# Performance work log

Hardware: AMD Instinct MI355X
Metric: run time of the kernel (lower is better)

Reference implementation:

```python
import jax, jax.numpy as jnp
import numpy as np

NEG = -9e15
SLOPE = 0.1  # LeakyReLU negative_slope in the torch module

B, N, NFEAT = 4, 2048, 256
NHID, NHEADS, NOUT = 64, 8, 128


def setup_inputs() -> dict:
    key = jax.random.key(0)
    ks = jax.random.split(key, 8)
    x = jax.random.normal(ks[0], (B, N, NFEAT), dtype=jnp.float32)
    adj = jax.random.randint(ks[1], (B, N, N), 0, 2, dtype=jnp.int32)
    s = 0.1
    Wh = jax.random.normal(ks[2], (NHEADS, NFEAT, NHID), dtype=jnp.float32) * s
    ah = jax.random.normal(ks[3], (NHEADS, 2 * NHID), dtype=jnp.float32) * s
    bh = jax.random.normal(ks[4], (NHEADS, NHID), dtype=jnp.float32) * s
    Wo = jax.random.normal(ks[5], (NHID * NHEADS, NOUT), dtype=jnp.float32) * s
    ao = jax.random.normal(ks[6], (2 * NOUT,), dtype=jnp.float32) * s
    bo = jax.random.normal(ks[7], (NOUT,), dtype=jnp.float32) * s
    return {"x": x, "adj": adj, "Wh": Wh, "ah": ah, "bh": bh,
            "Wo": Wo, "ao": ao, "bo": bo}


def _leaky(v):
    return jnp.where(v >= 0, v, SLOPE * v)


def _gat_layer(x, adj, W, a, b):
    # x: [B,N,Fin], W: [Fin,F], a: [2F], b: [F]
    h = jnp.einsum('bnf,fo->bno', x, W)          # [B,N,F]
    F = W.shape[1]
    a1, a2 = a[:F], a[F:]
    s1 = h @ a1                                   # [B,N] (query / row term)
    s2 = h @ a2                                   # [B,N] (key / col term)
    e = _leaky(s1[:, :, None] + s2[:, None, :])   # [B,N,N], avoids a_input blowup
    e = jnp.where(adj > 0, e, NEG)
    att = jax.nn.softmax(e, axis=2)               # [B,N,N]
    h_prime = jnp.einsum('bnm,bmf->bnf', att, h) + b
    return jax.nn.elu(h_prime)


def reference(x, adj, Wh, ah, bh, Wo, ao, bo):
    # per-head layers, vmapped over the head axis of the stacked params
    heads = jax.vmap(lambda W, a, b: _gat_layer(x, adj, W, a, b))(Wh, ah, bh)
    # [H,B,N,F] -> concat heads along feature dim: [B,N,H*F]
    hcat = jnp.transpose(heads, (1, 2, 0, 3)).reshape(x.shape[0], x.shape[1], -1)
    out = _gat_layer(hcat, adj, Wo, ao, bo)
    return jax.nn.relu(out)
```

## Files before the change

### kernel.cpp

```cpp
#include <hip/hip_runtime.h>

constexpr int B_ = 4;
constexpr int N_ = 2048;
constexpr int NFEAT_ = 256;
constexpr int NHEADS_ = 8;
constexpr float SLOPE_ = 0.1f;
constexpr float L2E = 1.4426950408889634f;

typedef __attribute__((ext_vector_type(8))) __fp16 f16x8;
typedef __attribute__((ext_vector_type(4))) __fp16 f16x4;
typedef __attribute__((ext_vector_type(2))) __fp16 f16x2;
typedef __attribute__((ext_vector_type(4))) float f32x4;
typedef __attribute__((ext_vector_type(2))) float f32x2;

__device__ __forceinline__ f16x8 pack8(const float* v) {
  union { f16x2 h2[4]; f16x8 h8; } u;
  u.h2[0] = __builtin_amdgcn_cvt_pkrtz(v[0], v[1]);
  u.h2[1] = __builtin_amdgcn_cvt_pkrtz(v[2], v[3]);
  u.h2[2] = __builtin_amdgcn_cvt_pkrtz(v[4], v[5]);
  u.h2[3] = __builtin_amdgcn_cvt_pkrtz(v[6], v[7]);
  return u.h8;
}
__device__ __forceinline__ f16x4 pack4(float a, float b, float c, float d) {
  union { f16x2 h2[2]; f16x4 h4; } u;
  u.h2[0] = __builtin_amdgcn_cvt_pkrtz(a, b);
  u.h2[1] = __builtin_amdgcn_cvt_pkrtz(c, d);
  return u.h4;
}

__device__ __forceinline__ unsigned int wpair(f32x2 p2, f32x2 s2p,
                                              f16x2 sl2, f16x2 cq2,
                                              unsigned int pm) {
  f32x2 z;
  asm("v_pk_add_f32 %0, %1, %2" : "=v"(z) : "v"(p2), "v"(s2p));
  f16x2 t0 = __builtin_amdgcn_cvt_pkrtz(z.x, z.y);
  f16x2 t1, tm;
  asm("v_pk_fma_f16 %0, %1, %2, %3" : "=v"(t1) : "v"(sl2), "v"(t0), "v"(cq2));
  asm("v_pk_max_f16 %0, %1, %2" : "=v"(tm) : "v"(t0), "v"(t1));
  unsigned int utm;
  __builtin_memcpy(&utm, &tm, 4);
  unsigned int hi, elo, ehi, pk;
  asm("v_lshrrev_b32 %0, 16, %1" : "=v"(hi) : "v"(utm));
  asm("v_exp_f16 %0, %1" : "=v"(elo) : "v"(utm));
  asm("v_exp_f16 %0, %1" : "=v"(ehi) : "v"(hi));
  asm("v_pack_b32_f16 %0, %1, %2" : "=v"(pk) : "v"(elo), "v"(ehi));
  return pk & pm;
}

__global__ __launch_bounds__(256) void k_prep(
    const int* __restrict__ adj, unsigned short* __restrict__ mask2,
    const float* __restrict__ Wh, __fp16* __restrict__ WhB,
    const float* __restrict__ Wo, __fp16* __restrict__ WoB)
{
  const int bid = blockIdx.x;
  const int l = threadIdx.x & 63;
  if (bid < 4096) {
    const size_t gw = ((size_t)bid * 256 + threadIdx.x) >> 6;
    const int jt = (int)(gw & 31);
    const int ig16 = (int)((gw >> 5) & 127);
    const int b = (int)(gw >> 12);
    const int q = l >> 4, c15 = l & 15;
    const int* base = adj + ((size_t)b * N_ + ig16 * 16) * N_ + jt * 64 + l;
    unsigned int msk = 0;
    #pragma unroll
    for (int r = 0; r < 16; ++r) {
      int a = base[(size_t)r * N_];
      unsigned long long bal = __ballot(a > 0);
      unsigned int v = (unsigned int)((bal >> (q * 8)) & 0xffull)
                     | ((unsigned int)((bal >> (q * 8 + 32)) & 0xffull) << 8);
      if (r == c15) msk = v;
    }
    mask2[gw * 64 + l] = (unsigned short)msk;
  } else if (bid < 4160) {
    int s = (int)(((bid - 4096) * 256 + threadIdx.x) >> 6);
    int h = s >> 5, ks = (s >> 2) & 7, ft = s & 3;
    const float* src = Wh + ((size_t)h * 256 + ks * 32 + (l >> 4) * 8) * 64 + ft * 16 + (l & 15);
    float v[8];
    #pragma unroll
    for (int j = 0; j < 8; ++j) v[j] = src[(size_t)j * 64];
    *(f16x8*)(WhB + (size_t)s * 512 + l * 8) = pack8(v);
  } else {
    int s = (int)(((bid - 4160) * 256 + threadIdx.x) >> 6);
    int ks = s >> 3, ft = s & 7;
    const float* src = Wo + ((size_t)ks * 32 + (l >> 4) * 8) * 128 + ft * 16 + (l & 15);
    float v[8];
    #pragma unroll
    for (int j = 0; j < 8; ++j) v[j] = src[(size_t)j * 128];
    *(f16x8*)(WoB + (size_t)s * 512 + l * 8) = pack8(v);
  }
}

__global__ __launch_bounds__(256, 4) void k_gemm1(
    const float* __restrict__ x, const __fp16* __restrict__ WhB,
    const float* __restrict__ ah,
    __fp16* __restrict__ hB1, float* __restrict__ s1h, float* __restrict__ s2h)
{
  constexpr int XP = 264;
  __shared__ __fp16 xs[16 * XP];
  __shared__ __fp16 hT[512 * 16];

  const int t = threadIdx.x;
  const int bid = blockIdx.x;
  const int b = bid >> 7;
  const int n0 = (bid & 127) * 16;

  {
    int r = t >> 4, k0 = (t & 15) * 16;
    const float* src = x + ((size_t)(b * N_) + n0 + r) * NFEAT_ + k0;
    float v0[8], v1[8];
    *(float4*)&v0[0] = *(const float4*)(src);
    *(float4*)&v0[4] = *(const float4*)(src + 4);
    *(float4*)&v1[0] = *(const float4*)(src + 8);
    *(float4*)&v1[4] = *(const float4*)(src + 12);
    *(f16x8*)&xs[r * XP + k0] = pack8(v0);
    *(f16x8*)&xs[r * XP + k0 + 8] = pack8(v1);
  }
  __syncthreads();

  const int w = t >> 6, l = t & 63;
  const int quad = l >> 4, c15 = l & 15;

  f32x4 acc[8];
  #pragma unroll
  for (int i = 0; i < 8; ++i) acc[i] = (f32x4){0.f, 0.f, 0.f, 0.f};

  for (int ks = 0; ks < 8; ++ks) {
    f16x8 af = *(const f16x8*)&xs[c15 * XP + ks * 32 + quad * 8];
    #pragma unroll
    for (int tt = 0; tt < 8; ++tt) {
      int hl = tt >> 2, ft = tt & 3;
      f16x8 bf = *(const f16x8*)(WhB +
          ((((size_t)(2 * w + hl) * 8 + ks) * 4 + ft) * 512) + l * 8);
      acc[tt] = __builtin_amdgcn_mfma_f32_16x16x32_f16(af, bf, acc[tt], 0, 0, 0);
    }
  }

  #pragma unroll
  for (int hl = 0; hl < 2; ++hl) {
    int head = 2 * w + hl;
    float a1v[4], a2v[4];
    #pragma unroll
    for (int ft = 0; ft < 4; ++ft) {
      a1v[ft] = ah[head * 128 + ft * 16 + c15] * L2E;
      a2v[ft] = ah[head * 128 + 64 + ft * 16 + c15] * L2E;
    }
    #pragma unroll
    for (int r = 0; r < 4; ++r) {
      float v1 = 0.f, v2 = 0.f;
      #pragma unroll
      for (int ft = 0; ft < 4; ++ft) {
        v1 = fmaf(acc[hl * 4 + ft][r], a1v[ft], v1);
        v2 = fmaf(acc[hl * 4 + ft][r], a2v[ft], v2);
      }
      #pragma unroll
      for (int off = 1; off < 16; off <<= 1) {
        v1 += __shfl_xor(v1, off, 64);
        v2 += __shfl_xor(v2, off, 64);
      }
      if (c15 == 0) {
        s1h[(size_t)(b * NHEADS_ + head) * N_ + n0 + quad * 4 + r] = v1;
        s2h[(size_t)(b * NHEADS_ + head) * N_ + n0 + quad * 4 + r] = v2;
      }
    }
  }

  #pragma unroll
  for (int tt = 0; tt < 8; ++tt) {
    int f = (2 * w + (tt >> 2)) * 64 + (tt & 3) * 16 + c15;
    *(f16x4*)&hT[f * 16 + quad * 4] =
        pack4(acc[tt][0], acc[tt][1], acc[tt][2], acc[tt][3]);
  }
  __syncthreads();

  const int base_oct = (n0 >> 3) & 3;
  #pragma unroll
  for (int q = 0; q < 4; ++q) {
    int s = t + q * 256;
    int c15v = s & 15, oct = (s >> 4) & 1, ft = (s >> 5) & 3, head = s >> 7;
    f16x8 v = *(const f16x8*)&hT[(head * 64 + ft * 16 + c15v) * 16 + oct * 8];
    int lane0 = (base_oct + oct) * 16 + c15v;
    *(f16x8*)(hB1 +
        ((((size_t)(b * NHEADS_ + head) * 64 + (n0 >> 5)) * 4 + ft) * 512) + lane0 * 8) = v;
  }
}

__global__ __launch_bounds__(256, 4) void k_gemm2(
    const __fp16* __restrict__ g1, const __fp16* __restrict__ WoB,
    const float* __restrict__ ao,
    __fp16* __restrict__ hB2, float* __restrict__ s1o, float* __restrict__ s2o)
{
  constexpr int GP = 520;
  __shared__ __fp16 gs[16 * GP];
  __shared__ __fp16 hT[128 * 16];
  __shared__ float sd1[4][16], sd2[4][16];

  const int t = threadIdx.x;
  const int bid = blockIdx.x;
  const int b = bid >> 7;
  const int n0 = (bid & 127) * 16;

  {
    int r = t >> 4, k0 = (t & 15) * 32;
    const __fp16* src = g1 + ((size_t)(b * N_) + n0 + r) * 512 + k0;
    #pragma unroll
    for (int i = 0; i < 4; ++i)
      *(f16x8*)&gs[r * GP + k0 + i * 8] = *(const f16x8*)(src + i * 8);
  }
  __syncthreads();

  const int w = t >> 6, l = t & 63;
  const int quad = l >> 4, c15 = l & 15;

  f32x4 acc[2];
  acc[0] = (f32x4){0.f, 0.f, 0.f, 0.f};
  acc[1] = (f32x4){0.f, 0.f, 0.f, 0.f};

  for (int ks = 0; ks < 16; ++ks) {
    f16x8 af = *(const f16x8*)&gs[c15 * GP + ks * 32 + quad * 8];
    #pragma unroll
    for (int tt = 0; tt < 2; ++tt) {
      int ft = 2 * w + tt;
      f16x8 bf = *(const f16x8*)(WoB + (((size_t)ks * 8 + ft) * 512) + l * 8);
      acc[tt] = __builtin_amdgcn_mfma_f32_16x16x32_f16(af, bf, acc[tt], 0, 0, 0);
    }
  }

  {
    float a1v[2], a2v[2];
    #pragma unroll
    for (int tt = 0; tt < 2; ++tt) {
      int f = (2 * w + tt) * 16 + c15;
      a1v[tt] = ao[f] * L2E;
      a2v[tt] = ao[128 + f] * L2E;
    }
    #pragma unroll
    for (int r = 0; r < 4; ++r) {
      float v1 = acc[0][r] * a1v[0] + acc[1][r] * a1v[1];
      float v2 = acc[0][r] * a2v[0] + acc[1][r] * a2v[1];
      #pragma unroll
      for (int off = 1; off < 16; off <<= 1) {
        v1 += __shfl_xor(v1, off, 64);
        v2 += __shfl_xor(v2, off, 64);
      }
      if (c15 == 0) { sd1[w][quad * 4 + r] = v1; sd2[w][quad * 4 + r] = v2; }
    }
  }

  #pragma unroll
  for (int tt = 0; tt < 2; ++tt) {
    int f = (2 * w + tt) * 16 + c15;
    *(f16x4*)&hT[f * 16 + quad * 4] =
        pack4(acc[tt][0], acc[tt][1], acc[tt][2], acc[tt][3]);
  }
  __syncthreads();

  if (t < 16)
    s1o[(size_t)b * N_ + n0 + t] = sd1[0][t] + sd1[1][t] + sd1[2][t] + sd1[3][t];
  else if (t < 32) {
    int rr = t - 16;
    s2o[(size_t)b * N_ + n0 + rr] = sd2[0][rr] + sd2[1][rr] + sd2[2][rr] + sd2[3][rr];
  }

  {
    int c15v = t & 15, oct = (t >> 4) & 1, ft = t >> 5;
    f16x8 v = *(const f16x8*)&hT[(ft * 16 + c15v) * 16 + oct * 8];
    int base_oct = (n0 >> 3) & 3;
    int lane0 = (base_oct + oct) * 16 + c15v;
    *(f16x8*)(hB2 +
        (((size_t)(b * 64 + (n0 >> 5)) * 8 + ft) * 512) + lane0 * 8) = v;
  }
}

__global__ __launch_bounds__(512, 4) void k_att1(
    const __fp16* __restrict__ hB, const float* __restrict__ s1,
    const float* __restrict__ s2, const unsigned short* __restrict__ mask2,
    const float* __restrict__ bias, __fp16* __restrict__ g1)
{
  constexpr int NRG = 4, NJQ = 2, JLEN = 1024, TJ = 32, NIT = JLEN / TJ;
  constexpr int TILE = TJ * 64;

  __shared__ __fp16 vbuf[NJQ][2][TILE];
  __shared__ float s2s[N_];
  __shared__ float red[8];
  __shared__ uint2 mlut[16];

  const int tid = threadIdx.x;
  const int w = tid >> 6, l = tid & 63;
  const int quad = l >> 4, c15 = l & 15;
  const int rowg = w % NRG, jq = w / NRG;
  const int tc = rowg * 64 + l;

  int idx = blockIdx.x;
  const int ig = idx & 31; idx >>= 5;
  const int head = idx & 7;
  const int b = idx >> 3;
  const int i0w = ig * 64 + rowg * 16;

  const float* s1p = s1 + (size_t)(b * 8 + head) * N_;
  const float* s2p = s2 + (size_t)(b * 8 + head) * N_;
  const char* hBp = (const char*)(hB + (size_t)(b * 8 + head) * (N_ / 32) * 2048);
  const unsigned short* mp = mask2 + ((size_t)(b * 128 + (i0w >> 4)) * 32) * 64 + l;

  const int jbase = jq * JLEN;

  if (tid < 16) {
    unsigned int v = tid;
    mlut[tid] = (uint2){ ((v & 1u) ? 0xffffu : 0u) | ((v & 2u) ? 0xffff0000u : 0u),
                         ((v & 4u) ? 0xffffu : 0u) | ((v & 8u) ? 0xffff0000u : 0u) };
  }

  float4 pf0 = *(const float4*)(hBp + (size_t)(jbase >> 5) * 4096 + tc * 16);
  unsigned short mk = mp[(size_t)(jbase >> 6) * 64];

  float4 sv = *(const float4*)(s2p + tid * 4);
  *(float4*)&s2s[tid * 4] = sv;
  float lm = fmaxf(fmaxf(sv.x, sv.y), fmaxf(sv.z, sv.w));
  #pragma unroll
  for (int off = 1; off < 64; off <<= 1) lm = fmaxf(lm, __shfl_xor(lm, off, 64));
  if (l == 0) red[w] = lm;
  const float s1v = s1p[i0w + c15];
  *(float4*)((char*)&vbuf[jq][0][0] + tc * 16) = pf0;
  __syncthreads();
  float s2m = red[0];
  #pragma unroll
  for (int q = 1; q < 8; ++q) s2m = fmaxf(s2m, red[q]);

  const float zm = s1v + s2m;
  const float m = fmaxf(zm, SLOPE_ * zm);
  const float p = s1v - m;
  const float cq = (SLOPE_ - 1.f) * m;
  const f16x2 cq2 = __builtin_amdgcn_cvt_pkrtz(cq, cq);
  const f16x2 sl2 = (f16x2){(__fp16)SLOPE_, (__fp16)SLOPE_};
  const f32x2 p2 = {p, p};

  f16x8 ones;
  #pragma unroll
  for (int i = 0; i < 8; ++i) ones[i] = (__fp16)1.0f;

  f32x4 acc[4], acc5;
  #pragma unroll
  for (int t = 0; t < 4; ++t) acc[t] = (f32x4){0.f, 0.f, 0.f, 0.f};
  acc5 = (f32x4){0.f, 0.f, 0.f, 0.f};

  for (int it = 0; it < NIT; ++it) {
    const int cur = it & 1;
    const int j0 = jbase + it * TJ;
    unsigned short nk = 0;
    float4 npf;
    if (it + 1 < NIT) {
      npf = *(const float4*)(hBp + (size_t)((j0 + TJ) >> 5) * 4096 + tc * 16);
      nk = mp[(size_t)((j0 + TJ) >> 6) * 64];
    }

    float4 sA = *(const float4*)&s2s[j0 + quad * 8];
    float4 sB = *(const float4*)&s2s[j0 + quad * 8 + 4];
    const unsigned int mbyte = ((unsigned int)mk >> (8 * ((j0 >> 5) & 1))) & 0xffu;
    const uint2 mA = mlut[mbyte & 15u];
    const uint2 mB = mlut[mbyte >> 4];
    union { unsigned int u[4]; f16x8 v8; } af;
    af.u[0] = wpair(p2, (f32x2){sA.x, sA.y}, sl2, cq2, mA.x);
    af.u[1] = wpair(p2, (f32x2){sA.z, sA.w}, sl2, cq2, mA.y);
    af.u[2] = wpair(p2, (f32x2){sB.x, sB.y}, sl2, cq2, mB.x);
    af.u[3] = wpair(p2, (f32x2){sB.z, sB.w}, sl2, cq2, mB.y);
    const f16x8 a = af.v8;
    acc5 = __builtin_amdgcn_mfma_f32_16x16x32_f16(a, ones, acc5, 0, 0, 0);
    const __fp16* vb = &vbuf[jq][cur][0];
    #pragma unroll
    for (int t = 0; t < 4; ++t) {
      f16x8 bf = *(const f16x8*)(vb + t * 512 + l * 8);
      acc[t] = __builtin_amdgcn_mfma_f32_16x16x32_f16(a, bf, acc[t], 0, 0, 0);
    }

    if (it + 1 < NIT) {
      *(float4*)((char*)&vbuf[jq][cur ^ 1][0] + tc * 16) = npf;
    }
    mk = nk;
    __syncthreads();
  }

  auto pacc = (float(*)[16][64])(&vbuf[0][0][0]);
  auto pls  = (float(*)[16])(&s2s[0]);
  if (jq == 1) {
    #pragma unroll
    for (int t = 0; t < 4; ++t)
      #pragma unroll
      for (int r = 0; r < 4; ++r)
        pacc[rowg][quad * 4 + r][t * 16 + c15] = acc[t][r];
    if (c15 == 0) {
      #pragma unroll
      for (int r = 0; r < 4; ++r) pls[rowg][quad * 4 + r] = acc5[r];
    }
  }
  __syncthreads();
  if (jq == 0) {
    float Lrow[4];
    #pragma unroll
    for (int r = 0; r < 4; ++r)
      Lrow[r] = acc5[r] + pls[rowg][quad * 4 + r];
    #pragma unroll
    for (int t = 0; t < 4; ++t)
      #pragma unroll
      for (int r = 0; r < 4; ++r)
        acc[t][r] += pacc[rowg][quad * 4 + r][t * 16 + c15];
    float lr[4];
    #pragma unroll
    for (int r = 0; r < 4; ++r) lr[r] = 1.f / Lrow[r];
    #pragma unroll
    for (int t = 0; t < 4; ++t) {
      const float bv = bias[head * 64 + t * 16 + c15];
      #pragma unroll
      for (int r = 0; r < 4; ++r) {
        const int i = i0w + quad * 4 + r;
        float v = acc[t][r] * lr[r] + bv;
        v = (v > 0.f) ? v : expm1f(v);
        g1[(size_t)(b * N_ + i) * 512 + head * 64 + t * 16 + c15] = (__fp16)v;
      }
    }
  }
}

__global__ __launch_bounds__(512, 4) void k_att2(
    const __fp16* __restrict__ hB, const float* __restrict__ s1,
    const float* __restrict__ s2, const unsigned short* __restrict__ mask2,
    const float* __restrict__ bias, float* __restrict__ out)
{
  constexpr int NRG = 2, NJQ = 4, JLEN = 512, TJ = 32, NIT = JLEN / TJ;
  constexpr int TILE = TJ * 64;

  __shared__ __fp16 vbuf[NJQ][2][TILE];
  __shared__ float s2s[N_];
  __shared__ float red[8];
  __shared__ uint2 mlut[16];

  const int tid = threadIdx.x;
  const int w = tid >> 6, l = tid & 63;
  const int quad = l >> 4, c15 = l & 15;
  const int rowg = w % NRG, jq = w / NRG;
  const int tc = rowg * 64 + l;

  int idx = blockIdx.x;
  const int ig = idx & 63; idx >>= 6;
  const int fs = idx & 1;
  const int b = idx >> 1;
  const int i0w = ig * 32 + rowg * 16;

  const float* s1p = s1 + (size_t)b * N_;
  const float* s2p = s2 + (size_t)b * N_;
  const char* hBp = (const char*)(hB + (size_t)b * 64 * 4096 + fs * 2048);
  const unsigned short* mp = mask2 + ((size_t)(b * 128 + (i0w >> 4)) * 32) * 64 + l;

  const int jbase = jq * JLEN;

  if (tid < 16) {
    unsigned int v = tid;
    mlut[tid] = (uint2){ ((v & 1u) ? 0xffffu : 0u) | ((v & 2u) ? 0xffff0000u : 0u),
                         ((v & 4u) ? 0xffffu : 0u) | ((v & 8u) ? 0xffff0000u : 0u) };
  }

  float4 pf0, pf1;
  {
    const char* srcb = hBp + (size_t)(jbase >> 5) * 8192;
    pf0 = *(const float4*)(srcb + tc * 16);
    pf1 = *(const float4*)(srcb + (tc + 128) * 16);
  }
  unsigned short mk = mp[(size_t)(jbase >> 6) * 64];

  float4 sv = *(const float4*)(s2p + tid * 4);
  *(float4*)&s2s[tid * 4] = sv;
  float lm = fmaxf(fmaxf(sv.x, sv.y), fmaxf(sv.z, sv.w));
  #pragma unroll
  for (int off = 1; off < 64; off <<= 1) lm = fmaxf(lm, __shfl_xor(lm, off, 64));
  if (l == 0) red[w] = lm;
  const float s1v = s1p[i0w + c15];
  *(float4*)((char*)&vbuf[jq][0][0] + tc * 16) = pf0;
  *(float4*)((char*)&vbuf[jq][0][0] + (tc + 128) * 16) = pf1;
  __syncthreads();
  float s2m = red[0];
  #pragma unroll
  for (int q = 1; q < 8; ++q) s2m = fmaxf(s2m, red[q]);

  const float zm = s1v + s2m;
  const float m = fmaxf(zm, SLOPE_ * zm);
  const float p = s1v - m;
  const float cq = (SLOPE_ - 1.f) * m;
  const f16x2 cq2 = __builtin_amdgcn_cvt_pkrtz(cq, cq);
  const f16x2 sl2 = (f16x2){(__fp16)SLOPE_, (__fp16)SLOPE_};
  const f32x2 p2 = {p, p};

  f16x8 ones;
  #pragma unroll
  for (int i = 0; i < 8; ++i) ones[i] = (__fp16)1.0f;

  f32x4 acc[4], acc5;
  #pragma unroll
  for (int t = 0; t < 4; ++t) acc[t] = (f32x4){0.f, 0.f, 0.f, 0.f};
  acc5 = (f32x4){0.f, 0.f, 0.f, 0.f};

  for (int it = 0; it < NIT; ++it) {
    const int cur = it & 1;
    const int j0 = jbase + it * TJ;
    unsigned short nk = 0;
    float4 npf0, npf1;
    if (it + 1 < NIT) {
      const char* srcb = hBp + (size_t)((j0 + TJ) >> 5) * 8192;
      npf0 = *(const float4*)(srcb + tc * 16);
      npf1 = *(const float4*)(srcb + (tc + 128) * 16);
      nk = mp[(size_t)((j0 + TJ) >> 6) * 64];
    }

    float4 sA = *(const float4*)&s2s[j0 + quad * 8];
    float4 sB = *(const float4*)&s2s[j0 + quad * 8 + 4];
    const unsigned int mbyte = ((unsigned int)mk >> (8 * ((j0 >> 5) & 1))) & 0xffu;
    const uint2 mA = mlut[mbyte & 15u];
    const uint2 mB = mlut[mbyte >> 4];
    union { unsigned int u[4]; f16x8 v8; } af;
    af.u[0] = wpair(p2, (f32x2){sA.x, sA.y}, sl2, cq2, mA.x);
    af.u[1] = wpair(p2, (f32x2){sA.z, sA.w}, sl2, cq2, mA.y);
    af.u[2] = wpair(p2, (f32x2){sB.x, sB.y}, sl2, cq2, mB.x);
    af.u[3] = wpair(p2, (f32x2){sB.z, sB.w}, sl2, cq2, mB.y);
    const f16x8 a = af.v8;
    acc5 = __builtin_amdgcn_mfma_f32_16x16x32_f16(a, ones, acc5, 0, 0, 0);
    const __fp16* vb = &vbuf[jq][cur][0];
    #pragma unroll
    for (int t = 0; t < 4; ++t) {
      f16x8 bf = *(const f16x8*)(vb + t * 512 + l * 8);
      acc[t] = __builtin_amdgcn_mfma_f32_16x16x32_f16(a, bf, acc[t], 0, 0, 0);
    }

    if (it + 1 < NIT) {
      char* dst = (char*)&vbuf[jq][cur ^ 1][0];
      *(float4*)(dst + tc * 16) = npf0;
      *(float4*)(dst + (tc + 128) * 16) = npf1;
    }
    mk = nk;
    __syncthreads();
  }

  auto pacc = (float(*)[NRG][16][64])(&vbuf[0][0][0]);
  auto pls  = (float(*)[NRG][16])(&s2s[0]);
  if (jq > 0) {
    #pragma unroll
    for (int t = 0; t < 4; ++t)
      #pragma unroll
      for (int r = 0; r < 4; ++r)
        pacc[jq - 1][rowg][quad * 4 + r][t * 16 + c15] = acc[t][r];
    if (c15 == 0) {
      #pragma unroll
      for (int r = 0; r < 4; ++r) pls[jq - 1][rowg][quad * 4 + r] = acc5[r];
    }
  }
  __syncthreads();
  if (jq == 0) {
    float Lrow[4];
    #pragma unroll
    for (int r = 0; r < 4; ++r) Lrow[r] = acc5[r];
    #pragma unroll
    for (int q = 0; q < NJQ - 1; ++q) {
      #pragma unroll
      for (int t = 0; t < 4; ++t)
        #pragma unroll
        for (int r = 0; r < 4; ++r)
          acc[t][r] += pacc[q][rowg][quad * 4 + r][t * 16 + c15];
      #pragma unroll
      for (int r = 0; r < 4; ++r) Lrow[r] += pls[q][rowg][quad * 4 + r];
    }
    float lr[4];
    #pragma unroll
    for (int r = 0; r < 4; ++r) lr[r] = 1.f / Lrow[r];
    #pragma unroll
    for (int t = 0; t < 4; ++t) {
      const float bv = bias[fs * 64 + t * 16 + c15];
      #pragma unroll
      for (int r = 0; r < 4; ++r) {
        const int i = i0w + quad * 4 + r;
        float v = acc[t][r] * lr[r] + bv;
        out[(size_t)(b * N_ + i) * 128 + fs * 64 + t * 16 + c15] = fmaxf(v, 0.f);
      }
    }
  }
}

extern "C" void kernel_launch(void* const* d_in, const int* in_sizes, int n_in,
                              void* d_out, int out_size, void* d_ws, size_t ws_size,
                              hipStream_t stream) {
  const float* x   = (const float*)d_in[0];
  const int*   adj = (const int*)d_in[1];
  const float* Wh  = (const float*)d_in[2];
  const float* ah  = (const float*)d_in[3];
  const float* bh  = (const float*)d_in[4];
  const float* Wo  = (const float*)d_in[5];
  const float* ao  = (const float*)d_in[6];
  const float* bo  = (const float*)d_in[7];
  float* out = (float*)d_out;

  float* ws   = (float*)d_ws;
  float* s1h  = ws;
  float* s2h  = s1h  + (size_t)B_ * NHEADS_ * N_;
  float* s1o  = s2h  + (size_t)B_ * NHEADS_ * N_;
  float* s2o  = s1o  + (size_t)B_ * N_;
  __fp16* g1  = (__fp16*)(s2o + (size_t)B_ * N_);
  __fp16* hB1 = g1  + (size_t)B_ * N_ * 512;
  __fp16* hB2 = hB1 + (size_t)B_ * NHEADS_ * N_ * 64;
  __fp16* WhB = hB2 + (size_t)B_ * N_ * 128;
  __fp16* WoB = WhB + (size_t)8 * 256 * 64;
  unsigned short* mask2 = (unsigned short*)(WoB + (size_t)512 * 128);

  k_prep<<<4192, 256, 0, stream>>>(adj, mask2, Wh, WhB, Wo, WoB);
  k_gemm1<<<B_ * (N_ / 16), 256, 0, stream>>>(x, WhB, ah, hB1, s1h, s2h);
  k_att1<<<B_ * NHEADS_ * (N_ / 64), 512, 0, stream>>>(
      hB1, s1h, s2h, mask2, bh, g1);
  k_gemm2<<<B_ * (N_ / 16), 256, 0, stream>>>(g1, WoB, ao, hB2, s1o, s2o);
  k_att2<<<B_ * 2 * (N_ / 32), 512, 0, stream>>>(
      hB2, s1o, s2o, mask2, bo, out);
}
```

Baseline: 194.0 us.

## Load attention value tiles directly from global into registers, drop LDS staging

Both attention kernels stop staging the hB value tiles through double-buffered shared memory with a barrier per tile. Each wave now loads its MFMA B-operands straight from global memory into registers, two tiles at a time with software prefetch. In k_att1 each wave covers the full key range for 16 rows, so the cross-wave reduction is gone and the grid is halved with 128 rows per block. This removes LDS traffic and __syncthreads stalls, but makes each wave re-read the same hB data from global/L2 and gives up the split-K parallelism in att1.

```diff
diff --git a/kernel.cpp b/kernel.cpp
--- a/kernel.cpp
+++ b/kernel.cpp
@@ -276,10 +276,8 @@
     const float* __restrict__ s2, const unsigned short* __restrict__ mask2,
     const float* __restrict__ bias, __fp16* __restrict__ g1)
 {
-  constexpr int NRG = 4, NJQ = 2, JLEN = 1024, TJ = 32, NIT = JLEN / TJ;
-  constexpr int TILE = TJ * 64;
-
-  __shared__ __fp16 vbuf[NJQ][2][TILE];
+  constexpr int NPR = N_ / 64;
+
   __shared__ float s2s[N_];
   __shared__ float red[8];
   __shared__ uint2 mlut[16];
@@ -287,21 +285,24 @@
   const int tid = threadIdx.x;
   const int w = tid >> 6, l = tid & 63;
   const int quad = l >> 4, c15 = l & 15;
-  const int rowg = w % NRG, jq = w / NRG;
-  const int tc = rowg * 64 + l;
 
   int idx = blockIdx.x;
-  const int ig = idx & 31; idx >>= 5;
+  const int ig = idx & 15; idx >>= 4;
   const int head = idx & 7;
   const int b = idx >> 3;
-  const int i0w = ig * 64 + rowg * 16;
+  const int i0w = ig * 128 + w * 16;
 
   const float* s1p = s1 + (size_t)(b * 8 + head) * N_;
   const float* s2p = s2 + (size_t)(b * 8 + head) * N_;
-  const char* hBp = (const char*)(hB + (size_t)(b * 8 + head) * (N_ / 32) * 2048);
+  const char* hBl = (const char*)(hB + (size_t)(b * 8 + head) * (N_ / 32) * 2048)
+                    + l * 16;
   const unsigned short* mp = mask2 + ((size_t)(b * 128 + (i0w >> 4)) * 32) * 64 + l;
 
-  const int jbase = jq * JLEN;
+  f16x8 bA[4], bB[4];
+  #pragma unroll
+  for (int t = 0; t < 4; ++t)
+    bA[t] = *(const f16x8*)(hBl + t * 1024);
+  unsigned short mk = mp[0];
 
   if (tid < 16) {
     unsigned int v = tid;
@@ -309,9 +310,6 @@
                          ((v & 4u) ? 0xffffu : 0u) | ((v & 8u) ? 0xffff0000u : 0u) };
   }
 
-  float4 pf0 = *(const float4*)(hBp + (size_t)(jbase >> 5) * 4096 + tc * 16);
-  unsigned short mk = mp[(size_t)(jbase >> 6) * 64];
-
   float4 sv = *(const float4*)(s2p + tid * 4);
   *(float4*)&s2s[tid * 4] = sv;
   float lm = fmaxf(fmaxf(sv.x, sv.y), fmaxf(sv.z, sv.w));
@@ -319,7 +317,6 @@
   for (int off = 1; off < 64; off <<= 1) lm = fmaxf(lm, __shfl_xor(lm, off, 64));
   if (l == 0) red[w] = lm;
   const float s1v = s1p[i0w + c15];
-  *(float4*)((char*)&vbuf[jq][0][0] + tc * 16) = pf0;
   __syncthreads();
   float s2m = red[0];
   #pragma unroll
@@ -342,79 +339,67 @@
   for (int t = 0; t < 4; ++t) acc[t] = (f32x4){0.f, 0.f, 0.f, 0.f};
   acc5 = (f32x4){0.f, 0.f, 0.f, 0.f};
 
-  for (int it = 0; it < NIT; ++it) {
-    const int cur = it & 1;
-    const int j0 = jbase + it * TJ;
+  for (int pr = 0; pr < NPR; ++pr) {
+    const int j0 = pr * 64;
+    #pragma unroll
+    for (int t = 0; t < 4; ++t)
+      bB[t] = *(const f16x8*)(hBl + (size_t)(j0 / 32 + 1) * 4096 + t * 1024);
+    {
+      float4 sA = *(const float4*)&s2s[j0 + quad * 8];
+      float4 sB = *(const float4*)&s2s[j0 + quad * 8 + 4];
+      const unsigned int mbyte = (unsigned int)mk & 0xffu;
+      const uint2 mA = mlut[mbyte & 15u];
+      const uint2 mH = mlut[mbyte >> 4];
+      union { unsigned int u[4]; f16x8 v8; } af;
+      af.u[0] = wpair(p2, (f32x2){sA.x, sA.y}, sl2, cq2, mA.x);
+      af.u[1] = wpair(p2, (f32x2){sA.z, sA.w}, sl2, cq2, mA.y);
+      af.u[2] = wpair(p2, (f32x2){sB.x, sB.y}, sl2, cq2, mH.x);
+      af.u[3] = wpair(p2, (f32x2){sB.z, sB.w}, sl2, cq2, mH.y);
+      const f16x8 a = af.v8;
+      acc5 = __builtin_amdgcn_mfma_f32_16x16x32_f16(a, ones, acc5, 0, 0, 0);
+      acc[0] = __builtin_amdgcn_mfma_f32_16x16x32_f16(a, bA[0], acc[0], 0, 0, 0);
+      acc[1] = __builtin_amdgcn_mfma_f32_16x16x32_f16(a, bA[1], acc[1], 0, 0, 0);
+      acc[2] = __builtin_amdgcn_mfma_f32_16x16x32_f16(a, bA[2], acc[2], 0, 0, 0);
+      acc[3] = __builtin_amdgcn_mfma_f32_16x16x32_f16(a, bA[3], acc[3], 0, 0, 0);
+    }
+    #pragma unroll
+    for (int t = 0; t < 4; ++t)
+      bA[t] = *(const f16x8*)(hBl + (size_t)(j0 / 32 + 2) * 4096 + t * 1024);
     unsigned short nk = 0;
-    float4 npf;
-    if (it + 1 < NIT) {
-      npf = *(const float4*)(hBp + (size_t)((j0 + TJ) >> 5) * 4096 + tc * 16);
-      nk = mp[(size_t)((j0 + TJ) >> 6) * 64];
-    }
-
-    float4 sA = *(const float4*)&s2s[j0 + quad * 8];
-    float4 sB = *(const float4*)&s2s[j0 + quad * 8 + 4];
-    const unsigned int mbyte = ((unsigned int)mk >> (8 * ((j0 >> 5) & 1))) & 0xffu;
-    const uint2 mA = mlut[mbyte & 15u];
-    const uint2 mB = mlut[mbyte >> 4];
-    union { unsigned int u[4]; f16x8 v8; } af;
-    af.u[0] = wpair(p2, (f32x2){sA.x, sA.y}, sl2, cq2, mA.x);
-    af.u[1] = wpair(p2, (f32x2){sA.z, sA.w}, sl2, cq2, mA.y);
-    af.u[2] = wpair(p2, (f32x2){sB.x, sB.y}, sl2, cq2, mB.x);
-    af.u[3] = wpair(p2, (f32x2){sB.z, sB.w}, sl2, cq2, mB.y);
-    const f16x8 a = af.v8;
-    acc5 = __builtin_amdgcn_mfma_f32_16x16x32_f16(a, ones, acc5, 0, 0, 0);
-    const __fp16* vb = &vbuf[jq][cur][0];
-    #pragma unroll
-    for (int t = 0; t < 4; ++t) {
-      f16x8 bf = *(const f16x8*)(vb + t * 512 + l * 8);
-      acc[t] = __builtin_amdgcn_mfma_f32_16x16x32_f16(a, bf, acc[t], 0, 0, 0);
-    }
-
-    if (it + 1 < NIT) {
-      *(float4*)((char*)&vbuf[jq][cur ^ 1][0] + tc * 16) = npf;
+    if (pr + 1 < NPR) nk = mp[(size_t)(pr + 1) * 64];
+    {
+      float4 sA = *(const float4*)&s2s[j0 + 32 + quad * 8];
+      float4 sB = *(const float4*)&s2s[j0 + 32 + quad * 8 + 4];
+      const unsigned int mbyte = ((unsigned int)mk >> 8) & 0xffu;
+      const uint2 mA = mlut[mbyte & 15u];
+      const uint2 mH = mlut[mbyte >> 4];
+      union { unsigned int u[4]; f16x8 v8; } af;
+      af.u[0] = wpair(p2, (f32x2){sA.x, sA.y}, sl2, cq2, mA.x);
+      af.u[1] = wpair(p2, (f32x2){sA.z, sA.w}, sl2, cq2, mA.y);
+      af.u[2] = wpair(p2, (f32x2){sB.x, sB.y}, sl2, cq2, mH.x);
+      af.u[3] = wpair(p2, (f32x2){sB.z, sB.w}, sl2, cq2, mH.y);
+      const f16x8 a = af.v8;
+      acc5 = __builtin_amdgcn_mfma_f32_16x16x32_f16(a, ones, acc5, 0, 0, 0);
+      acc[0] = __builtin_amdgcn_mfma_f32_16x16x32_f16(a, bB[0], acc[0], 0, 0, 0);
+      acc[1] = __builtin_amdgcn_mfma_f32_16x16x32_f16(a, bB[1], acc[1], 0, 0, 0);
+      acc[2] = __builtin_amdgcn_mfma_f32_16x16x32_f16(a, bB[2], acc[2], 0, 0, 0);
+      acc[3] = __builtin_amdgcn_mfma_f32_16x16x32_f16(a, bB[3], acc[3], 0, 0, 0);
     }
     mk = nk;
-    __syncthreads();
-  }
-
-  auto pacc = (float(*)[16][64])(&vbuf[0][0][0]);
-  auto pls  = (float(*)[16])(&s2s[0]);
-  if (jq == 1) {
-    #pragma unroll
-    for (int t = 0; t < 4; ++t)
-      #pragma unroll
-      for (int r = 0; r < 4; ++r)
-        pacc[rowg][quad * 4 + r][t * 16 + c15] = acc[t][r];
-    if (c15 == 0) {
-      #pragma unroll
-      for (int r = 0; r < 4; ++r) pls[rowg][quad * 4 + r] = acc5[r];
-    }
-  }
-  __syncthreads();
-  if (jq == 0) {
-    float Lrow[4];
-    #pragma unroll
-    for (int r = 0; r < 4; ++r)
-      Lrow[r] = acc5[r] + pls[rowg][quad * 4 + r];
-    #pragma unroll
-    for (int t = 0; t < 4; ++t)
-      #pragma unroll
-      for (int r = 0; r < 4; ++r)
-        acc[t][r] += pacc[rowg][quad * 4 + r][t * 16 + c15];
-    float lr[4];
-    #pragma unroll
-    for (int r = 0; r < 4; ++r) lr[r] = 1.f / Lrow[r];
-    #pragma unroll
-    for (int t = 0; t < 4; ++t) {
-      const float bv = bias[head * 64 + t * 16 + c15];
-      #pragma unroll
-      for (int r = 0; r < 4; ++r) {
-        const int i = i0w + quad * 4 + r;
-        float v = acc[t][r] * lr[r] + bv;
-        v = (v > 0.f) ? v : expm1f(v);
-        g1[(size_t)(b * N_ + i) * 512 + head * 64 + t * 16 + c15] = (__fp16)v;
-      }
+  }
+
+  float lr[4];
+  #pragma unroll
+  for (int r = 0; r < 4; ++r) lr[r] = 1.f / acc5[r];
+  #pragma unroll
+  for (int t = 0; t < 4; ++t) {
+    const float bv = bias[head * 64 + t * 16 + c15];
+    #pragma unroll
+    for (int r = 0; r < 4; ++r) {
+      const int i = i0w + quad * 4 + r;
+      float v = acc[t][r] * lr[r] + bv;
+      v = (v > 0.f) ? v : expm1f(v);
+      g1[(size_t)(b * N_ + i) * 512 + head * 64 + t * 16 + c15] = (__fp16)v;
     }
   }
 }
@@ -424,19 +409,18 @@
     const float* __restrict__ s2, const unsigned short* __restrict__ mask2,
     const float* __restrict__ bias, float* __restrict__ out)
 {
-  constexpr int NRG = 2, NJQ = 4, JLEN = 512, TJ = 32, NIT = JLEN / TJ;
-  constexpr int TILE = TJ * 64;
-
-  __shared__ __fp16 vbuf[NJQ][2][TILE];
+  constexpr int NRG = 2, NJQ = 4, JLEN = 512, NPR = JLEN / 64;
+
   __shared__ float s2s[N_];
   __shared__ float red[8];
   __shared__ uint2 mlut[16];
+  __shared__ float pacc[NJQ - 1][NRG][16][64];
+  __shared__ float pls[NJQ - 1][NRG][16];
 
   const int tid = threadIdx.x;
   const int w = tid >> 6, l = tid & 63;
   const int quad = l >> 4, c15 = l & 15;
   const int rowg = w % NRG, jq = w / NRG;
-  const int tc = rowg * 64 + l;
 
   int idx = blockIdx.x;
   const int ig = idx & 63; idx >>= 6;
@@ -446,10 +430,17 @@
 
   const float* s1p = s1 + (size_t)b * N_;
   const float* s2p = s2 + (size_t)b * N_;
-  const char* hBp = (const char*)(hB + (size_t)b * 64 * 4096 + fs * 2048);
+  const char* hBl = (const char*)(hB + (size_t)b * 64 * 4096 + fs * 2048) + l * 16;
   const unsigned short* mp = mask2 + ((size_t)(b * 128 + (i0w >> 4)) * 32) * 64 + l;
 
   const int jbase = jq * JLEN;
+  const int tbase = jbase / 32;
+
+  f16x8 bA[4], bB[4];
+  #pragma unroll
+  for (int t = 0; t < 4; ++t)
+    bA[t] = *(const f16x8*)(hBl + (size_t)tbase * 8192 + t * 1024);
+  unsigned short mk = mp[(size_t)(jbase >> 6) * 64];
 
   if (tid < 16) {
     unsigned int v = tid;
@@ -457,14 +448,6 @@
                          ((v & 4u) ? 0xffffu : 0u) | ((v & 8u) ? 0xffff0000u : 0u) };
   }
 
-  float4 pf0, pf1;
-  {
-    const char* srcb = hBp + (size_t)(jbase >> 5) * 8192;
-    pf0 = *(const float4*)(srcb + tc * 16);
-    pf1 = *(const float4*)(srcb + (tc + 128) * 16);
-  }
-  unsigned short mk = mp[(size_t)(jbase >> 6) * 64];
-
   float4 sv = *(const float4*)(s2p + tid * 4);
   *(float4*)&s2s[tid * 4] = sv;
   float lm = fmaxf(fmaxf(sv.x, sv.y), fmaxf(sv.z, sv.w));
@@ -472,8 +455,6 @@
   for (int off = 1; off < 64; off <<= 1) lm = fmaxf(lm, __shfl_xor(lm, off, 64));
   if (l == 0) red[w] = lm;
   const float s1v = s1p[i0w + c15];
-  *(float4*)((char*)&vbuf[jq][0][0] + tc * 16) = pf0;
-  *(float4*)((char*)&vbuf[jq][0][0] + (tc + 128) * 16) = pf1;
   __syncthreads();
   float s2m = red[0];
   #pragma unroll
@@ -496,48 +477,55 @@
   for (int t = 0; t < 4; ++t) acc[t] = (f32x4){0.f, 0.f, 0.f, 0.f};
   acc5 = (f32x4){0.f, 0.f, 0.f, 0.f};
 
-  for (int it = 0; it < NIT; ++it) {
-    const int cur = it & 1;
-    const int j0 = jbase + it * TJ;
+  for (int pr = 0; pr < NPR; ++pr) {
+    const int j0 = jbase + pr * 64;
+    #pragma unroll
+    for (int t = 0; t < 4; ++t)
+      bB[t] = *(const f16x8*)(hBl + (size_t)(j0 / 32 + 1) * 8192 + t * 1024);
+    {
+      float4 sA = *(const float4*)&s2s[j0 + quad * 8];
+      float4 sB = *(const float4*)&s2s[j0 + quad * 8 + 4];
+      const unsigned int mbyte = (unsigned int)mk & 0xffu;
+      const uint2 mA = mlut[mbyte & 15u];
+      const uint2 mH = mlut[mbyte >> 4];
+      union { unsigned int u[4]; f16x8 v8; } af;
+      af.u[0] = wpair(p2, (f32x2){sA.x, sA.y}, sl2, cq2, mA.x);
+      af.u[1] = wpair(p2, (f32x2){sA.z, sA.w}, sl2, cq2, mA.y);
+      af.u[2] = wpair(p2, (f32x2){sB.x, sB.y}, sl2, cq2, mH.x);
+      af.u[3] = wpair(p2, (f32x2){sB.z, sB.w}, sl2, cq2, mH.y);
+      const f16x8 a = af.v8;
+      acc5 = __builtin_amdgcn_mfma_f32_16x16x32_f16(a, ones, acc5, 0, 0, 0);
+      acc[0] = __builtin_amdgcn_mfma_f32_16x16x32_f16(a, bA[0], acc[0], 0, 0, 0);
+      acc[1] = __builtin_amdgcn_mfma_f32_16x16x32_f16(a, bA[1], acc[1], 0, 0, 0);
+      acc[2] = __builtin_amdgcn_mfma_f32_16x16x32_f16(a, bA[2], acc[2], 0, 0, 0);
+      acc[3] = __builtin_amdgcn_mfma_f32_16x16x32_f16(a, bA[3], acc[3], 0, 0, 0);
+    }
+    #pragma unroll
+    for (int t = 0; t < 4; ++t)
+      bA[t] = *(const f16x8*)(hBl + (size_t)(j0 / 32 + 2) * 8192 + t * 1024);
     unsigned short nk = 0;
-    float4 npf0, npf1;
-    if (it + 1 < NIT) {
-      const char* srcb = hBp + (size_t)((j0 + TJ) >> 5) * 8192;
-      npf0 = *(const float4*)(srcb + tc * 16);
-      npf1 = *(const float4*)(srcb + (tc + 128) * 16);
-      nk = mp[(size_t)((j0 + TJ) >> 6) * 64];
-    }
-
-    float4 sA = *(const float4*)&s2s[j0 + quad * 8];
-    float4 sB = *(const float4*)&s2s[j0 + quad * 8 + 4];
-    const unsigned int mbyte = ((unsigned int)mk >> (8 * ((j0 >> 5) & 1))) & 0xffu;
-    const uint2 mA = mlut[mbyte & 15u];
-    const uint2 mB = mlut[mbyte >> 4];
-    union { unsigned int u[4]; f16x8 v8; } af;
-    af.u[0] = wpair(p2, (f32x2){sA.x, sA.y}, sl2, cq2, mA.x);
-    af.u[1] = wpair(p2, (f32x2){sA.z, sA.w}, sl2, cq2, mA.y);
-    af.u[2] = wpair(p2, (f32x2){sB.x, sB.y}, sl2, cq2, mB.x);
-    af.u[3] = wpair(p2, (f32x2){sB.z, sB.w}, sl2, cq2, mB.y);
-    const f16x8 a = af.v8;
-    acc5 = __builtin_amdgcn_mfma_f32_16x16x32_f16(a, ones, acc5, 0, 0, 0);
-    const __fp16* vb = &vbuf[jq][cur][0];
-    #pragma unroll
-    for (int t = 0; t < 4; ++t) {
-      f16x8 bf = *(const f16x8*)(vb + t * 512 + l * 8);
-      acc[t] = __builtin_amdgcn_mfma_f32_16x16x32_f16(a, bf, acc[t], 0, 0, 0);
-    }
-
-    if (it + 1 < NIT) {
-      char* dst = (char*)&vbuf[jq][cur ^ 1][0];
-      *(float4*)(dst + tc * 16) = npf0;
-      *(float4*)(dst + (tc + 128) * 16) = npf1;
+    if (pr + 1 < NPR) nk = mp[(size_t)((j0 + 64) >> 6) * 64];
+    {
+      float4 sA = *(const float4*)&s2s[j0 + 32 + quad * 8];
+      float4 sB = *(const float4*)&s2s[j0 + 32 + quad * 8 + 4];
+      const unsigned int mbyte = ((unsigned int)mk >> 8) & 0xffu;
+      const uint2 mA = mlut[mbyte & 15u];
+      const uint2 mH = mlut[mbyte >> 4];
+      union { unsigned int u[4]; f16x8 v8; } af;
+      af.u[0] = wpair(p2, (f32x2){sA.x, sA.y}, sl2, cq2, mA.x);
+      af.u[1] = wpair(p2, (f32x2){sA.z, sA.w}, sl2, cq2, mA.y);
+      af.u[2] = wpair(p2, (f32x2){sB.x, sB.y}, sl2, cq2, mH.x);
+      af.u[3] = wpair(p2, (f32x2){sB.z, sB.w}, sl2, cq2, mH.y);
+      const f16x8 a = af.v8;
+      acc5 = __builtin_amdgcn_mfma_f32_16x16x32_f16(a, ones, acc5, 0, 0, 0);
+      acc[0] = __builtin_amdgcn_mfma_f32_16x16x32_f16(a, bB[0], acc[0], 0, 0, 0);
+      acc[1] = __builtin_amdgcn_mfma_f32_16x16x32_f16(a, bB[1], acc[1], 0, 0, 0);
+      acc[2] = __builtin_amdgcn_mfma_f32_16x16x32_f16(a, bB[2], acc[2], 0, 0, 0);
+      acc[3] = __builtin_amdgcn_mfma_f32_16x16x32_f16(a, bB[3], acc[3], 0, 0, 0);
     }
     mk = nk;
-    __syncthreads();
-  }
-
-  auto pacc = (float(*)[NRG][16][64])(&vbuf[0][0][0]);
-  auto pls  = (float(*)[NRG][16])(&s2s[0]);
+  }
+
   if (jq > 0) {
     #pragma unroll
     for (int t = 0; t < 4; ++t)
@@ -607,7 +595,7 @@
 
   k_prep<<<4192, 256, 0, stream>>>(adj, mask2, Wh, WhB, Wo, WoB);
   k_gemm1<<<B_ * (N_ / 16), 256, 0, stream>>>(x, WhB, ah, hB1, s1h, s2h);
-  k_att1<<<B_ * NHEADS_ * (N_ / 64), 512, 0, stream>>>(
+  k_att1<<<B_ * NHEADS_ * (N_ / 128), 512, 0, stream>>>(
       hB1, s1h, s2h, mask2, bh, g1);
   k_gemm2<<<B_ * (N_ / 16), 256, 0, stream>>>(g1, WoB, ao, hB2, s1o, s2o);
   k_att2<<<B_ * 2 * (N_ / 32), 512, 0, stream>>>(
```

Result: no change. 191.8 us (-1.1%).
